# Kernel optimization log

Hardware: AMD Instinct MI355X
Metric: run time of the kernel (lower is better)

## Reference

```python
import jax, jax.numpy as jnp
import numpy as np

N = 50000
E = 800000
D = 128
L = 2


def setup_inputs() -> dict:
    key = jax.random.key(0)
    k0, k1, k2 = jax.random.split(key, 3)
    x = jax.random.normal(k0, (N, D), dtype=jnp.float32)
    edge_index = jax.random.randint(k1, (2, E), 0, N, dtype=jnp.int64)
    # GCNConv weights: one [D, D] matrix + bias per layer (dim_in -> dim_in)
    W = jax.random.normal(k2, (L, D, D), dtype=jnp.float32) * (1.0 / np.sqrt(D))
    b = jnp.zeros((L, D), dtype=jnp.float32)
    return {"x": x, "edge_index": edge_index, "W": W, "b": b}


def reference(x, edge_index, W, b):
    """Stacked GCNConv + relu (dropout is identity in eval mode).

    GCNConv: out = D^{-1/2} (A + I) D^{-1/2} (X W) + b, with self-loops added.
    """
    n = x.shape[0]
    loops = jnp.arange(n, dtype=edge_index.dtype)
    src = jnp.concatenate([edge_index[0], loops])  # [E + N]
    dst = jnp.concatenate([edge_index[1], loops])  # [E + N]
    # Degree (with self-loops) based symmetric normalization
    deg = jax.ops.segment_sum(jnp.ones_like(dst, dtype=x.dtype), dst, num_segments=n)
    dinv = jax.lax.rsqrt(deg)  # deg >= 1 thanks to self-loops
    coef = (dinv[src] * dinv[dst])[:, None]  # [E + N, 1]

    num_layers = W.shape[0]
    for i in range(num_layers):
        h = x @ W[i]  # transform first, as PyG GCNConv does
        x = jax.ops.segment_sum(h[src] * coef, dst, num_segments=n) + b[i]
        x = jax.nn.relu(x)
        # F.dropout with training=False is identity
    return x
```

## Files before the change

kernel.cpp:

```cpp
#include <hip/hip_runtime.h>
#include <hip/hip_fp16.h>


#define D 128
#define SCAN_B 256
#define WP 136
#define ABI 6

typedef _Float16 half8 __attribute__((ext_vector_type(8)));
typedef float floatx4 __attribute__((ext_vector_type(4)));


__global__ void count_kernel(const int* __restrict__ dst, int* deg8,
                             int* __restrict__ rank, int e, int n) {
    int i = blockIdx.x * blockDim.x + threadIdx.x;
    int c = (blockIdx.x & 7) * n;
    if (i < e) rank[i] = atomicAdd(&deg8[c + dst[i]], 1);
}

__global__ __launch_bounds__(256) void scanA_cvtw_kernel(const int* __restrict__ deg8,
                                                         int* __restrict__ degT,
                                                         int* __restrict__ base8,
                                                         int* __restrict__ partial,
                                                         int n, int nbs,
                                                         const float* __restrict__ W,
                                                         __half* __restrict__ WhT) {
    __shared__ int red[4];
    int tid = threadIdx.x;
    int bid = blockIdx.x;
    if (bid < nbs) {
        int i = bid * 256 + tid;
        int tot = 0;
        if (i < n) {
            int run = 0;
#pragma unroll
            for (int c = 0; c < 8; ++c) {
                base8[c * n + i] = run;
                run += deg8[c * n + i];
            }
            degT[i] = run;
            tot = run;
        }
        for (int off = 32; off > 0; off >>= 1) tot += __shfl_down(tot, off, 64);
        if ((tid & 63) == 0) red[tid >> 6] = tot;
        __syncthreads();
        if (tid == 0) partial[bid] = red[0] + red[1] + red[2] + red[3];
    } else {
        int id = (bid - nbs) * 256 + tid;
        int l = id >> 14;
        int rem = id & 16383;
        int f = rem >> 7;
        int k = rem & 127;
        WhT[id] = __float2half(W[l * 16384 + k * 128 + f]);
    }
}

__global__ __launch_bounds__(256) void scanB_kernel(const int* __restrict__ partial,
                                                    int* __restrict__ blockoff, int nb) {
    __shared__ int sc[256];
    int tid = threadIdx.x;
    int c = (tid < nb) ? partial[tid] : 0;
    sc[tid] = c;
    __syncthreads();
    for (int off = 1; off < 256; off <<= 1) {
        int v = (tid >= off) ? sc[tid - off] : 0;
        __syncthreads();
        sc[tid] += v;
        __syncthreads();
    }
    if (tid <= nb) blockoff[tid] = (tid == 0) ? 0 : sc[tid - 1];
}

__global__ __launch_bounds__(SCAN_B) void scanC_kernel(const int* __restrict__ degT,
                                                       const int* __restrict__ blockoff,
                                                       int* __restrict__ row_ptr,
                                                       float* __restrict__ dinv,
                                                       int n, int nb) {
    __shared__ int sc[SCAN_B];
    int tid = threadIdx.x;
    int i = blockIdx.x * SCAN_B + tid;
    int c = (i < n) ? degT[i] : 0;
    sc[tid] = c;
    __syncthreads();
    for (int off = 1; off < SCAN_B; off <<= 1) {
        int v = (tid >= off) ? sc[tid - off] : 0;
        __syncthreads();
        sc[tid] += v;
        __syncthreads();
    }
    if (i < n) {
        int base = blockoff[blockIdx.x] + sc[tid] - c;
        row_ptr[i] = base;
        dinv[i] = rsqrtf((float)(c + 1));
    }
    if (blockIdx.x == 0 && tid == 0) row_ptr[n] = blockoff[nb];
}


__device__ inline void gemm_body(int bid, int tid,
                                 const float* __restrict__ Xf,
                                 const __half* __restrict__ Xh,
                                 const __half* __restrict__ WhT,
                                 __half* __restrict__ Hh, int n, int fromFloat,
                                 _Float16* wlds) {
#pragma unroll
    for (int q = 0; q < 8; ++q) {
        int idx = tid + q * 256;
        int row = idx >> 4;
        int col8 = (idx & 15) * 8;
        const uint2* gsrc = (const uint2*)(WhT + row * 128 + col8);
        uint2 a = gsrc[0];
        uint2 b = gsrc[1];
        uint2* ldst = (uint2*)(wlds + row * WP + col8);
        ldst[0] = a;
        ldst[1] = b;
    }
    __syncthreads();

    const int wave = tid >> 6;
    const int lane = tid & 63;
    const int m = lane & 15;
    const int quad = lane >> 4;

    const int node = bid * 64 + wave * 16 + m;
    const int node_ld = node < n ? node : (n - 1);

    half8 bfr[4];
    if (fromFloat) {
#pragma unroll
        for (int k = 0; k < 4; ++k) {
            const float4* p = (const float4*)(Xf + (size_t)node_ld * 128 + k * 32 + quad * 8);
            float4 lo = p[0];
            float4 hi = p[1];
            half8 h;
            h[0] = (_Float16)lo.x; h[1] = (_Float16)lo.y;
            h[2] = (_Float16)lo.z; h[3] = (_Float16)lo.w;
            h[4] = (_Float16)hi.x; h[5] = (_Float16)hi.y;
            h[6] = (_Float16)hi.z; h[7] = (_Float16)hi.w;
            bfr[k] = h;
        }
    } else {
#pragma unroll
        for (int k = 0; k < 4; ++k) {
            bfr[k] = *(const half8*)(Xh + (size_t)node_ld * 128 + k * 32 + quad * 8);
        }
    }

    floatx4 acc[8];
#pragma unroll
    for (int f = 0; f < 8; ++f) acc[f] = (floatx4){0.f, 0.f, 0.f, 0.f};

#pragma unroll
    for (int f = 0; f < 8; ++f) {
#pragma unroll
        for (int k = 0; k < 4; ++k) {
            half8 a = *(const half8*)(wlds + (f * 16 + m) * WP + k * 32 + quad * 8);
            acc[f] = __builtin_amdgcn_mfma_f32_16x16x32_f16(a, bfr[k], acc[f], 0, 0, 0);
        }
    }

    if (node < n) {
#pragma unroll
        for (int f = 0; f < 8; ++f) {
            __half2 p0 = __floats2half2_rn(acc[f][0], acc[f][1]);
            __half2 p1 = __floats2half2_rn(acc[f][2], acc[f][3]);
            uint2 pk;
            pk.x = *(unsigned int*)&p0;
            pk.y = *(unsigned int*)&p1;
            *(uint2*)(Hh + (size_t)node * 128 + f * 16 + quad * 4) = pk;
        }
    }
}

__device__ inline void fill_body(int i,
                                 const int* __restrict__ src,
                                 const int* __restrict__ dst,
                                 const int* __restrict__ rank,
                                 const int* __restrict__ row_ptr,
                                 const int* __restrict__ base8,
                                 const float* __restrict__ dinv,
                                 int2* __restrict__ recs, int e, int n) {
    if (i < e) {
        int d = dst[i];
        int s = src[i];
        int c = (i >> 8) & 7;
        int pos = row_ptr[d] + base8[c * n + d] + rank[i];
        int2 rec;
        rec.x = s;
        rec.y = __float_as_int(dinv[s] * dinv[d]);
        recs[pos] = rec;
    }
}


__global__ __launch_bounds__(256) void gemmfill_kernel(const float* __restrict__ Xf,
                                                       const __half* __restrict__ WhT,
                                                       __half* __restrict__ Hh, int n, int nbg,
                                                       const int* __restrict__ src,
                                                       const int* __restrict__ dst,
                                                       const int* __restrict__ rank,
                                                       const int* __restrict__ row_ptr,
                                                       const int* __restrict__ base8,
                                                       const float* __restrict__ dinv,
                                                       int2* __restrict__ recs, int e) {
    __shared__ _Float16 wlds[128 * WP];
    int bid = blockIdx.x;
    int tid = threadIdx.x;
    if (bid < nbg) {
        gemm_body(bid, tid, Xf, nullptr, WhT, Hh, n, 1, wlds);
    } else {
        fill_body((bid - nbg) * 256 + tid, src, dst, rank, row_ptr, base8, dinv, recs, e, n);
    }
}

__global__ __launch_bounds__(256) void gemm_f16in_kernel(const __half* __restrict__ Xh,
                                                         const __half* __restrict__ WhT,
                                                         __half* __restrict__ Hh, int n) {
    __shared__ _Float16 wlds[128 * WP];
    gemm_body(blockIdx.x, threadIdx.x, nullptr, Xh, WhT, Hh, n, 0, wlds);
}


__device__ inline void unpack8(uint4 u, float* f) {
    union { unsigned int x; __half2 h; } a, b, c, d;
    a.x = u.x; b.x = u.y; c.x = u.z; d.x = u.w;
    float2 f0 = __half22float2(a.h);
    float2 f1 = __half22float2(b.h);
    float2 f2 = __half22float2(c.h);
    float2 f3 = __half22float2(d.h);
    f[0] = f0.x; f[1] = f0.y; f[2] = f1.x; f[3] = f1.y;
    f[4] = f2.x; f[5] = f2.y; f[6] = f3.x; f[7] = f3.y;
}

__global__ __launch_bounds__(256) void agg_kernel(const __half* __restrict__ H,
                                                  const int2* __restrict__ recs,
                                                  const int* __restrict__ row_ptr,
                                                  const float* __restrict__ dinv,
                                                  const float* __restrict__ bias,
                                                  float* __restrict__ YF,
                                                  __half* __restrict__ YH,
                                                  int n, int writeHalf) {
    int wave = threadIdx.x >> 6;
    int lane = threadIdx.x & 63;
    int v = blockIdx.x * 4 + wave;
    if (v >= n) return;

    const int qw = lane >> 4;
    const int fl = lane & 15;
    const uint4* H16 = (const uint4*)H;

    float acc[8];
    {
        float di = dinv[v];
        float selfc = (qw == 0) ? di * di : 0.f;
        uint4 hv = H16[(size_t)v * 16 + fl];
        float f[8]; unpack8(hv, f);
#pragma unroll
        for (int t = 0; t < 8; ++t) acc[t] = f[t] * selfc;
    }

    int e0 = row_ptr[v];
    int e1 = row_ptr[v + 1];
    int e = e0;
    for (; e + 4 * ABI <= e1; e += 4 * ABI) {
        int2 r[ABI]; uint4 hu[ABI];
#pragma unroll
        for (int j = 0; j < ABI; ++j) r[j] = recs[e + 4 * j + qw];
#pragma unroll
        for (int j = 0; j < ABI; ++j) hu[j] = H16[(size_t)r[j].x * 16 + fl];
#pragma unroll
        for (int j = 0; j < ABI; ++j) {
            float c = __int_as_float(r[j].y);
            float f[8]; unpack8(hu[j], f);
#pragma unroll
            for (int t = 0; t < 8; ++t) acc[t] = fmaf(f[t], c, acc[t]);
        }
    }
    if (e < e1) {
        int2 r[ABI]; uint4 hu[ABI]; bool act[ABI];
#pragma unroll
        for (int j = 0; j < ABI; ++j) {
            int idx = e + 4 * j + qw;
            act[j] = idx < e1;
            if (act[j]) r[j] = recs[idx];
        }
#pragma unroll
        for (int j = 0; j < ABI; ++j) {
            if (act[j]) hu[j] = H16[(size_t)r[j].x * 16 + fl];
        }
#pragma unroll
        for (int j = 0; j < ABI; ++j) {
            if (act[j]) {
                float c = __int_as_float(r[j].y);
                float f[8]; unpack8(hu[j], f);
#pragma unroll
                for (int t = 0; t < 8; ++t) acc[t] = fmaf(f[t], c, acc[t]);
            }
        }
    }

#pragma unroll
    for (int t = 0; t < 8; ++t) {
        acc[t] += __shfl_xor(acc[t], 16);
        acc[t] += __shfl_xor(acc[t], 32);
    }

    if (qw == 0) {
        const float4* B4 = (const float4*)bias;
        float4 b0 = B4[fl * 2];
        float4 b1 = B4[fl * 2 + 1];
        float o[8];
        o[0] = fmaxf(acc[0] + b0.x, 0.f);
        o[1] = fmaxf(acc[1] + b0.y, 0.f);
        o[2] = fmaxf(acc[2] + b0.z, 0.f);
        o[3] = fmaxf(acc[3] + b0.w, 0.f);
        o[4] = fmaxf(acc[4] + b1.x, 0.f);
        o[5] = fmaxf(acc[5] + b1.y, 0.f);
        o[6] = fmaxf(acc[6] + b1.z, 0.f);
        o[7] = fmaxf(acc[7] + b1.w, 0.f);
        if (writeHalf) {
            __half2 p0 = __floats2half2_rn(o[0], o[1]);
            __half2 p1 = __floats2half2_rn(o[2], o[3]);
            __half2 p2 = __floats2half2_rn(o[4], o[5]);
            __half2 p3 = __floats2half2_rn(o[6], o[7]);
            uint4 pk;
            pk.x = *(unsigned int*)&p0;
            pk.y = *(unsigned int*)&p1;
            pk.z = *(unsigned int*)&p2;
            pk.w = *(unsigned int*)&p3;
            ((uint4*)YH)[(size_t)v * 16 + fl] = pk;
        } else {
            float4* Y4 = (float4*)YF;
            Y4[(size_t)v * 32 + fl * 2]     = make_float4(o[0], o[1], o[2], o[3]);
            Y4[(size_t)v * 32 + fl * 2 + 1] = make_float4(o[4], o[5], o[6], o[7]);
        }
    }
}


extern "C" void kernel_launch(void* const* d_in, const int* in_sizes, int n_in,
                              void* d_out, int out_size, void* d_ws, size_t ws_size,
                              hipStream_t stream) {
    const float* x = (const float*)d_in[0];
    const int* ei = (const int*)d_in[1];
    const float* W = (const float*)d_in[2];
    const float* b = (const float*)d_in[3];
    float* out = (float*)d_out;

    const int N = in_sizes[0] / D;
    const int E = in_sizes[1] / 2;

    const int* src = ei;
    const int* dst = ei + E;

    int* wsi = (int*)d_ws;
    float* wsf = (float*)d_ws;
    const size_t o_deg8 = 0;
    const size_t o_degT = o_deg8 + 400000;
    const size_t o_dinv = o_degT + 50000;
    const size_t o_rp   = o_dinv + 50000;
    const size_t o_part = o_rp + 50016;
    const size_t o_boff = o_part + 256;
    const size_t o_b8   = o_boff + 256;
    const size_t o_rank = o_b8 + 400000;
    const size_t o_rec  = o_rank + 800000;
    const size_t o_h    = o_rec + 1600000;
    const size_t o_wht  = o_h + 3200000;
    const size_t o_y1h  = o_wht + 16384;

    int* deg8    = wsi + o_deg8;
    int* degT    = wsi + o_degT;
    float* dinv  = wsf + o_dinv;
    int* row_ptr = wsi + o_rp;
    int* partial = wsi + o_part;
    int* blockoff= wsi + o_boff;
    int* base8   = wsi + o_b8;
    int* rank    = wsi + o_rank;
    int2* recs   = (int2*)(wsi + o_rec);
    __half* h    = (__half*)(wsi + o_h);
    __half* wht  = (__half*)(wsi + o_wht);
    __half* y1h  = (__half*)(wsi + o_y1h);

    const int nb_e = (E + 255) / 256;
    const int nb_s = (N + SCAN_B - 1) / SCAN_B;
    const int nb_g = (N + 63) / 64;
    const int nb_a = (N + 3) / 4;

    hipMemsetAsync(deg8, 0, (size_t)8 * 50000 * sizeof(int), stream);
    count_kernel<<<nb_e, 256, 0, stream>>>(dst, deg8, rank, E, N);
    scanA_cvtw_kernel<<<nb_s + 128, 256, 0, stream>>>(deg8, degT, base8, partial,
                                                      N, nb_s, W, wht);
    scanB_kernel<<<1, 256, 0, stream>>>(partial, blockoff, nb_s);
    scanC_kernel<<<nb_s, SCAN_B, 0, stream>>>(degT, blockoff, row_ptr, dinv, N, nb_s);
    gemmfill_kernel<<<nb_g + nb_e, 256, 0, stream>>>(x, wht, h, N, nb_g,
                                                     src, dst, rank, row_ptr, base8,
                                                     dinv, recs, E);
    agg_kernel<<<nb_a, 256, 0, stream>>>(h, recs, row_ptr, dinv, b, nullptr, y1h, N, 1);
    gemm_f16in_kernel<<<nb_g, 256, 0, stream>>>(y1h, wht + 16384, h, N);
    agg_kernel<<<nb_a, 256, 0, stream>>>(h, recs, row_ptr, dinv, b + D, out, nullptr, N, 0);
}
```

Before: 238.4 us.

## Fuse deg zeroing with weight conversion, overlap first GEMM with edge counting

Replaces the memset with a zeroing kernel that also converts W to fp16 transposed. The first-layer GEMM now runs in the same launch as the atomic degree count instead of alongside the CSR fill, so the fill becomes its own kernel. This reorders the preprocessing schedule to hide the GEMM behind the atomic-bound count phase and removes one launch. In exchange, the count blocks now share a launch with GEMM blocks that need large LDS, which may limit occupancy for the atomic work.

```diff
diff --git a/kernel.cpp b/kernel.cpp
--- a/kernel.cpp
+++ b/kernel.cpp
@@ -11,48 +11,144 @@
 typedef float floatx4 __attribute__((ext_vector_type(4)));
 
 
-__global__ void count_kernel(const int* __restrict__ dst, int* deg8,
-                             int* __restrict__ rank, int e, int n) {
-    int i = blockIdx.x * blockDim.x + threadIdx.x;
-    int c = (blockIdx.x & 7) * n;
-    if (i < e) rank[i] = atomicAdd(&deg8[c + dst[i]], 1);
-}
-
-__global__ __launch_bounds__(256) void scanA_cvtw_kernel(const int* __restrict__ deg8,
-                                                         int* __restrict__ degT,
-                                                         int* __restrict__ base8,
-                                                         int* __restrict__ partial,
-                                                         int n, int nbs,
-                                                         const float* __restrict__ W,
-                                                         __half* __restrict__ WhT) {
-    __shared__ int red[4];
+__global__ __launch_bounds__(256) void zero_cvtw_kernel(int* __restrict__ deg8,
+                                                        int total4, int nzb,
+                                                        const float* __restrict__ W,
+                                                        __half* __restrict__ WhT) {
+    int bid = blockIdx.x;
     int tid = threadIdx.x;
-    int bid = blockIdx.x;
-    if (bid < nbs) {
+    if (bid < nzb) {
         int i = bid * 256 + tid;
-        int tot = 0;
-        if (i < n) {
-            int run = 0;
-#pragma unroll
-            for (int c = 0; c < 8; ++c) {
-                base8[c * n + i] = run;
-                run += deg8[c * n + i];
-            }
-            degT[i] = run;
-            tot = run;
-        }
-        for (int off = 32; off > 0; off >>= 1) tot += __shfl_down(tot, off, 64);
-        if ((tid & 63) == 0) red[tid >> 6] = tot;
-        __syncthreads();
-        if (tid == 0) partial[bid] = red[0] + red[1] + red[2] + red[3];
+        if (i < total4) ((int4*)deg8)[i] = make_int4(0, 0, 0, 0);
     } else {
-        int id = (bid - nbs) * 256 + tid;
+        int id = (bid - nzb) * 256 + tid;
         int l = id >> 14;
         int rem = id & 16383;
         int f = rem >> 7;
         int k = rem & 127;
         WhT[id] = __float2half(W[l * 16384 + k * 128 + f]);
     }
+}
+
+
+__device__ inline void gemm_body(int bid, int tid,
+                                 const float* __restrict__ Xf,
+                                 const __half* __restrict__ Xh,
+                                 const __half* __restrict__ WhT,
+                                 __half* __restrict__ Hh, int n, int fromFloat,
+                                 _Float16* wlds) {
+#pragma unroll
+    for (int q = 0; q < 8; ++q) {
+        int idx = tid + q * 256;
+        int row = idx >> 4;
+        int col8 = (idx & 15) * 8;
+        const uint2* gsrc = (const uint2*)(WhT + row * 128 + col8);
+        uint2 a = gsrc[0];
+        uint2 b = gsrc[1];
+        uint2* ldst = (uint2*)(wlds + row * WP + col8);
+        ldst[0] = a;
+        ldst[1] = b;
+    }
+    __syncthreads();
+
+    const int wave = tid >> 6;
+    const int lane = tid & 63;
+    const int m = lane & 15;
+    const int quad = lane >> 4;
+
+    const int node = bid * 64 + wave * 16 + m;
+    const int node_ld = node < n ? node : (n - 1);
+
+    half8 bfr[4];
+    if (fromFloat) {
+#pragma unroll
+        for (int k = 0; k < 4; ++k) {
+            const float4* p = (const float4*)(Xf + (size_t)node_ld * 128 + k * 32 + quad * 8);
+            float4 lo = p[0];
+            float4 hi = p[1];
+            half8 h;
+            h[0] = (_Float16)lo.x; h[1] = (_Float16)lo.y;
+            h[2] = (_Float16)lo.z; h[3] = (_Float16)lo.w;
+            h[4] = (_Float16)hi.x; h[5] = (_Float16)hi.y;
+            h[6] = (_Float16)hi.z; h[7] = (_Float16)hi.w;
+            bfr[k] = h;
+        }
+    } else {
+#pragma unroll
+        for (int k = 0; k < 4; ++k) {
+            bfr[k] = *(const half8*)(Xh + (size_t)node_ld * 128 + k * 32 + quad * 8);
+        }
+    }
+
+    floatx4 acc[8];
+#pragma unroll
+    for (int f = 0; f < 8; ++f) acc[f] = (floatx4){0.f, 0.f, 0.f, 0.f};
+
+#pragma unroll
+    for (int f = 0; f < 8; ++f) {
+#pragma unroll
+        for (int k = 0; k < 4; ++k) {
+            half8 a = *(const half8*)(wlds + (f * 16 + m) * WP + k * 32 + quad * 8);
+            acc[f] = __builtin_amdgcn_mfma_f32_16x16x32_f16(a, bfr[k], acc[f], 0, 0, 0);
+        }
+    }
+
+    if (node < n) {
+#pragma unroll
+        for (int f = 0; f < 8; ++f) {
+            __half2 p0 = __floats2half2_rn(acc[f][0], acc[f][1]);
+            __half2 p1 = __floats2half2_rn(acc[f][2], acc[f][3]);
+            uint2 pk;
+            pk.x = *(unsigned int*)&p0;
+            pk.y = *(unsigned int*)&p1;
+            *(uint2*)(Hh + (size_t)node * 128 + f * 16 + quad * 4) = pk;
+        }
+    }
+}
+
+
+__global__ __launch_bounds__(256) void count_gemm_kernel(const int* __restrict__ dst,
+                                                         int* deg8,
+                                                         int* __restrict__ rank,
+                                                         int e, int n, int nbe,
+                                                         const float* __restrict__ Xf,
+                                                         const __half* __restrict__ WhT,
+                                                         __half* __restrict__ Hh) {
+    __shared__ _Float16 wlds[128 * WP];
+    int bid = blockIdx.x;
+    int tid = threadIdx.x;
+    if (bid < nbe) {
+        int i = bid * 256 + tid;
+        int c = (bid & 7) * n;
+        if (i < e) rank[i] = atomicAdd(&deg8[c + dst[i]], 1);
+    } else {
+        gemm_body(bid - nbe, tid, Xf, nullptr, WhT, Hh, n, 1, wlds);
+    }
+}
+
+
+__global__ __launch_bounds__(256) void scanA_kernel(const int* __restrict__ deg8,
+                                                    int* __restrict__ degT,
+                                                    int* __restrict__ base8,
+                                                    int* __restrict__ partial, int n) {
+    __shared__ int red[4];
+    int tid = threadIdx.x;
+    int i = blockIdx.x * 256 + tid;
+    int tot = 0;
+    if (i < n) {
+        int run = 0;
+#pragma unroll
+        for (int c = 0; c < 8; ++c) {
+            base8[c * n + i] = run;
+            run += deg8[c * n + i];
+        }
+        degT[i] = run;
+        tot = run;
+    }
+    for (int off = 32; off > 0; off >>= 1) tot += __shfl_down(tot, off, 64);
+    if ((tid & 63) == 0) red[tid >> 6] = tot;
+    __syncthreads();
+    if (tid == 0) partial[blockIdx.x] = red[0] + red[1] + red[2] + red[3];
 }
 
 __global__ __launch_bounds__(256) void scanB_kernel(const int* __restrict__ partial,
@@ -97,89 +193,13 @@
 }
 
 
-__device__ inline void gemm_body(int bid, int tid,
-                                 const float* __restrict__ Xf,
-                                 const __half* __restrict__ Xh,
-                                 const __half* __restrict__ WhT,
-                                 __half* __restrict__ Hh, int n, int fromFloat,
-                                 _Float16* wlds) {
-#pragma unroll
-    for (int q = 0; q < 8; ++q) {
-        int idx = tid + q * 256;
-        int row = idx >> 4;
-        int col8 = (idx & 15) * 8;
-        const uint2* gsrc = (const uint2*)(WhT + row * 128 + col8);
-        uint2 a = gsrc[0];
-        uint2 b = gsrc[1];
-        uint2* ldst = (uint2*)(wlds + row * WP + col8);
-        ldst[0] = a;
-        ldst[1] = b;
-    }
-    __syncthreads();
-
-    const int wave = tid >> 6;
-    const int lane = tid & 63;
-    const int m = lane & 15;
-    const int quad = lane >> 4;
-
-    const int node = bid * 64 + wave * 16 + m;
-    const int node_ld = node < n ? node : (n - 1);
-
-    half8 bfr[4];
-    if (fromFloat) {
-#pragma unroll
-        for (int k = 0; k < 4; ++k) {
-            const float4* p = (const float4*)(Xf + (size_t)node_ld * 128 + k * 32 + quad * 8);
-            float4 lo = p[0];
-            float4 hi = p[1];
-            half8 h;
-            h[0] = (_Float16)lo.x; h[1] = (_Float16)lo.y;
-            h[2] = (_Float16)lo.z; h[3] = (_Float16)lo.w;
-            h[4] = (_Float16)hi.x; h[5] = (_Float16)hi.y;
-            h[6] = (_Float16)hi.z; h[7] = (_Float16)hi.w;
-            bfr[k] = h;
-        }
-    } else {
-#pragma unroll
-        for (int k = 0; k < 4; ++k) {
-            bfr[k] = *(const half8*)(Xh + (size_t)node_ld * 128 + k * 32 + quad * 8);
-        }
-    }
-
-    floatx4 acc[8];
-#pragma unroll
-    for (int f = 0; f < 8; ++f) acc[f] = (floatx4){0.f, 0.f, 0.f, 0.f};
-
-#pragma unroll
-    for (int f = 0; f < 8; ++f) {
-#pragma unroll
-        for (int k = 0; k < 4; ++k) {
-            half8 a = *(const half8*)(wlds + (f * 16 + m) * WP + k * 32 + quad * 8);
-            acc[f] = __builtin_amdgcn_mfma_f32_16x16x32_f16(a, bfr[k], acc[f], 0, 0, 0);
-        }
-    }
-
-    if (node < n) {
-#pragma unroll
-        for (int f = 0; f < 8; ++f) {
-            __half2 p0 = __floats2half2_rn(acc[f][0], acc[f][1]);
-            __half2 p1 = __floats2half2_rn(acc[f][2], acc[f][3]);
-            uint2 pk;
-            pk.x = *(unsigned int*)&p0;
-            pk.y = *(unsigned int*)&p1;
-            *(uint2*)(Hh + (size_t)node * 128 + f * 16 + quad * 4) = pk;
-        }
-    }
-}
-
-__device__ inline void fill_body(int i,
-                                 const int* __restrict__ src,
-                                 const int* __restrict__ dst,
-                                 const int* __restrict__ rank,
-                                 const int* __restrict__ row_ptr,
-                                 const int* __restrict__ base8,
-                                 const float* __restrict__ dinv,
-                                 int2* __restrict__ recs, int e, int n) {
+__global__ void fill_kernel(const int* __restrict__ src, const int* __restrict__ dst,
+                            const int* __restrict__ rank,
+                            const int* __restrict__ row_ptr,
+                            const int* __restrict__ base8,
+                            const float* __restrict__ dinv,
+                            int2* __restrict__ recs, int e, int n) {
+    int i = blockIdx.x * blockDim.x + threadIdx.x;
     if (i < e) {
         int d = dst[i];
         int s = src[i];
@@ -192,26 +212,6 @@
     }
 }
 
-
-__global__ __launch_bounds__(256) void gemmfill_kernel(const float* __restrict__ Xf,
-                                                       const __half* __restrict__ WhT,
-                                                       __half* __restrict__ Hh, int n, int nbg,
-                                                       const int* __restrict__ src,
-                                                       const int* __restrict__ dst,
-                                                       const int* __restrict__ rank,
-                                                       const int* __restrict__ row_ptr,
-                                                       const int* __restrict__ base8,
-                                                       const float* __restrict__ dinv,
-                                                       int2* __restrict__ recs, int e) {
-    __shared__ _Float16 wlds[128 * WP];
-    int bid = blockIdx.x;
-    int tid = threadIdx.x;
-    if (bid < nbg) {
-        gemm_body(bid, tid, Xf, nullptr, WhT, Hh, n, 1, wlds);
-    } else {
-        fill_body((bid - nbg) * 256 + tid, src, dst, rank, row_ptr, base8, dinv, recs, e, n);
-    }
-}
 
 __global__ __launch_bounds__(256) void gemm_f16in_kernel(const __half* __restrict__ Xh,
                                                          const __half* __restrict__ WhT,
@@ -385,16 +385,15 @@
     const int nb_s = (N + SCAN_B - 1) / SCAN_B;
     const int nb_g = (N + 63) / 64;
     const int nb_a = (N + 3) / 4;
-
-    hipMemsetAsync(deg8, 0, (size_t)8 * 50000 * sizeof(int), stream);
-    count_kernel<<<nb_e, 256, 0, stream>>>(dst, deg8, rank, E, N);
-    scanA_cvtw_kernel<<<nb_s + 128, 256, 0, stream>>>(deg8, degT, base8, partial,
-                                                      N, nb_s, W, wht);
+    const int nzb  = (100000 + 255) / 256;
+
+    zero_cvtw_kernel<<<nzb + 128, 256, 0, stream>>>(deg8, 100000, nzb, W, wht);
+    count_gemm_kernel<<<nb_e + nb_g, 256, 0, stream>>>(dst, deg8, rank, E, N, nb_e,
+                                                       x, wht, h);
+    scanA_kernel<<<nb_s, 256, 0, stream>>>(deg8, degT, base8, partial, N);
     scanB_kernel<<<1, 256, 0, stream>>>(partial, blockoff, nb_s);
     scanC_kernel<<<nb_s, SCAN_B, 0, stream>>>(degT, blockoff, row_ptr, dinv, N, nb_s);
-    gemmfill_kernel<<<nb_g + nb_e, 256, 0, stream>>>(x, wht, h, N, nb_g,
-                                                     src, dst, rank, row_ptr, base8,
-                                                     dinv, recs, E);
+    fill_kernel<<<nb_e, 256, 0, stream>>>(src, dst, rank, row_ptr, base8, dinv, recs, E, N);
     agg_kernel<<<nb_a, 256, 0, stream>>>(h, recs, row_ptr, dinv, b, nullptr, y1h, N, 1);
     gemm_f16in_kernel<<<nb_g, 256, 0, stream>>>(y1h, wht + 16384, h, N);
     agg_kernel<<<nb_a, 256, 0, stream>>>(h, recs, row_ptr, dinv, b + D, out, nullptr, N, 0);
```

After: 240.1 us. About the same (+0.8%).

## Slice feature matrix into 16-column panels and split aggregation across slices

Applied to the files above, without the earlier changes.

The intermediate H and Y1 matrices are stored as eight column slices of 16 halves each (slice-major), written that way by the GEMM and read that way by the next GEMM. Aggregation now launches eight blocks per node group, each handling one 16-column slice, so each gathered row is a 32-byte segment from a slice that is 1.6MB. The intent is to make each slice's working set cache-resident and raise edge-level parallelism. The cost is that the edge records are re-read eight times per node and there are more, smaller gathers.

```diff
diff --git a/kernel.cpp b/kernel.cpp
--- a/kernel.cpp
+++ b/kernel.cpp
@@ -5,7 +5,7 @@
 #define D 128
 #define SCAN_B 256
 #define WP 136
-#define ABI 6
+#define AB2 4
 
 typedef _Float16 half8 __attribute__((ext_vector_type(8)));
 typedef float floatx4 __attribute__((ext_vector_type(4)));
@@ -142,7 +142,8 @@
     } else {
 #pragma unroll
         for (int k = 0; k < 4; ++k) {
-            bfr[k] = *(const half8*)(Xh + (size_t)node_ld * 128 + k * 32 + quad * 8);
+            int sl = 2 * k + (quad >> 1);
+            bfr[k] = *(const half8*)(Xh + ((size_t)sl * n + node_ld) * 16 + (quad & 1) * 8);
         }
     }
 
@@ -167,7 +168,7 @@
             uint2 pk;
             pk.x = *(unsigned int*)&p0;
             pk.y = *(unsigned int*)&p1;
-            *(uint2*)(Hh + (size_t)node * 128 + f * 16 + quad * 4) = pk;
+            *(uint2*)(Hh + ((size_t)f * n + node) * 16 + quad * 4) = pk;
         }
     }
 }
@@ -221,17 +222,6 @@
 }
 
 
-__device__ inline void unpack8(uint4 u, float* f) {
-    union { unsigned int x; __half2 h; } a, b, c, d;
-    a.x = u.x; b.x = u.y; c.x = u.z; d.x = u.w;
-    float2 f0 = __half22float2(a.h);
-    float2 f1 = __half22float2(b.h);
-    float2 f2 = __half22float2(c.h);
-    float2 f3 = __half22float2(d.h);
-    f[0] = f0.x; f[1] = f0.y; f[2] = f1.x; f[3] = f1.y;
-    f[4] = f2.x; f[5] = f2.y; f[6] = f3.x; f[7] = f3.y;
-}
-
 __global__ __launch_bounds__(256) void agg_kernel(const __half* __restrict__ H,
                                                   const int2* __restrict__ recs,
                                                   const int* __restrict__ row_ptr,
@@ -242,97 +232,84 @@
                                                   int n, int writeHalf) {
     int wave = threadIdx.x >> 6;
     int lane = threadIdx.x & 63;
-    int v = blockIdx.x * 4 + wave;
+    int s = blockIdx.x & 7;
+    int v = (blockIdx.x >> 3) * 4 + wave;
     if (v >= n) return;
 
-    const int qw = lane >> 4;
-    const int fl = lane & 15;
-    const uint4* H16 = (const uint4*)H;
-
-    float acc[8];
+    const int eo = lane >> 3;
+    const int fl = lane & 7;
+    const unsigned int* Hu = (const unsigned int*)H;
+    const size_t sbase = (size_t)s * n;
+
+    float ax, ay;
     {
         float di = dinv[v];
-        float selfc = (qw == 0) ? di * di : 0.f;
-        uint4 hv = H16[(size_t)v * 16 + fl];
-        float f[8]; unpack8(hv, f);
-#pragma unroll
-        for (int t = 0; t < 8; ++t) acc[t] = f[t] * selfc;
+        float selfc = (eo == 0) ? di * di : 0.f;
+        union { unsigned int u; __half2 h; } cv;
+        cv.u = Hu[(sbase + v) * 8 + fl];
+        float2 hv = __half22float2(cv.h);
+        ax = hv.x * selfc;
+        ay = hv.y * selfc;
     }
 
     int e0 = row_ptr[v];
     int e1 = row_ptr[v + 1];
+    const unsigned long long* rec8 = (const unsigned long long*)recs;
     int e = e0;
-    for (; e + 4 * ABI <= e1; e += 4 * ABI) {
-        int2 r[ABI]; uint4 hu[ABI];
-#pragma unroll
-        for (int j = 0; j < ABI; ++j) r[j] = recs[e + 4 * j + qw];
-#pragma unroll
-        for (int j = 0; j < ABI; ++j) hu[j] = H16[(size_t)r[j].x * 16 + fl];
-#pragma unroll
-        for (int j = 0; j < ABI; ++j) {
-            float c = __int_as_float(r[j].y);
-            float f[8]; unpack8(hu[j], f);
-#pragma unroll
-            for (int t = 0; t < 8; ++t) acc[t] = fmaf(f[t], c, acc[t]);
+    for (; e + 8 * AB2 <= e1; e += 8 * AB2) {
+        unsigned long long r[AB2]; unsigned int hu[AB2];
+#pragma unroll
+        for (int j = 0; j < AB2; ++j)
+            r[j] = __builtin_nontemporal_load(rec8 + e + 8 * j + eo);
+#pragma unroll
+        for (int j = 0; j < AB2; ++j)
+            hu[j] = Hu[(sbase + (unsigned int)(r[j] & 0xffffffffu)) * 8 + fl];
+#pragma unroll
+        for (int j = 0; j < AB2; ++j) {
+            float c = __int_as_float((int)(r[j] >> 32));
+            union { unsigned int u; __half2 h; } t; t.u = hu[j];
+            float2 hs = __half22float2(t.h);
+            ax = fmaf(hs.x, c, ax);
+            ay = fmaf(hs.y, c, ay);
         }
     }
     if (e < e1) {
-        int2 r[ABI]; uint4 hu[ABI]; bool act[ABI];
-#pragma unroll
-        for (int j = 0; j < ABI; ++j) {
-            int idx = e + 4 * j + qw;
+        unsigned long long r[AB2]; unsigned int hu[AB2]; bool act[AB2];
+#pragma unroll
+        for (int j = 0; j < AB2; ++j) {
+            int idx = e + 8 * j + eo;
             act[j] = idx < e1;
-            if (act[j]) r[j] = recs[idx];
-        }
-#pragma unroll
-        for (int j = 0; j < ABI; ++j) {
-            if (act[j]) hu[j] = H16[(size_t)r[j].x * 16 + fl];
-        }
-#pragma unroll
-        for (int j = 0; j < ABI; ++j) {
+            if (act[j]) r[j] = __builtin_nontemporal_load(rec8 + idx);
+        }
+#pragma unroll
+        for (int j = 0; j < AB2; ++j) {
+            if (act[j]) hu[j] = Hu[(sbase + (unsigned int)(r[j] & 0xffffffffu)) * 8 + fl];
+        }
+#pragma unroll
+        for (int j = 0; j < AB2; ++j) {
             if (act[j]) {
-                float c = __int_as_float(r[j].y);
-                float f[8]; unpack8(hu[j], f);
-#pragma unroll
-                for (int t = 0; t < 8; ++t) acc[t] = fmaf(f[t], c, acc[t]);
+                float c = __int_as_float((int)(r[j] >> 32));
+                union { unsigned int u; __half2 h; } t; t.u = hu[j];
+                float2 hs = __half22float2(t.h);
+                ax = fmaf(hs.x, c, ax);
+                ay = fmaf(hs.y, c, ay);
             }
         }
     }
 
-#pragma unroll
-    for (int t = 0; t < 8; ++t) {
-        acc[t] += __shfl_xor(acc[t], 16);
-        acc[t] += __shfl_xor(acc[t], 32);
-    }
-
-    if (qw == 0) {
-        const float4* B4 = (const float4*)bias;
-        float4 b0 = B4[fl * 2];
-        float4 b1 = B4[fl * 2 + 1];
-        float o[8];
-        o[0] = fmaxf(acc[0] + b0.x, 0.f);
-        o[1] = fmaxf(acc[1] + b0.y, 0.f);
-        o[2] = fmaxf(acc[2] + b0.z, 0.f);
-        o[3] = fmaxf(acc[3] + b0.w, 0.f);
-        o[4] = fmaxf(acc[4] + b1.x, 0.f);
-        o[5] = fmaxf(acc[5] + b1.y, 0.f);
-        o[6] = fmaxf(acc[6] + b1.z, 0.f);
-        o[7] = fmaxf(acc[7] + b1.w, 0.f);
+    ax += __shfl_xor(ax, 8);  ay += __shfl_xor(ay, 8);
+    ax += __shfl_xor(ax, 16); ay += __shfl_xor(ay, 16);
+    ax += __shfl_xor(ax, 32); ay += __shfl_xor(ay, 32);
+
+    if (eo == 0) {
+        float2 bv = ((const float2*)bias)[s * 8 + fl];
+        float ox = fmaxf(ax + bv.x, 0.f);
+        float oy = fmaxf(ay + bv.y, 0.f);
         if (writeHalf) {
-            __half2 p0 = __floats2half2_rn(o[0], o[1]);
-            __half2 p1 = __floats2half2_rn(o[2], o[3]);
-            __half2 p2 = __floats2half2_rn(o[4], o[5]);
-            __half2 p3 = __floats2half2_rn(o[6], o[7]);
-            uint4 pk;
-            pk.x = *(unsigned int*)&p0;
-            pk.y = *(unsigned int*)&p1;
-            pk.z = *(unsigned int*)&p2;
-            pk.w = *(unsigned int*)&p3;
-            ((uint4*)YH)[(size_t)v * 16 + fl] = pk;
+            __half2 p = __floats2half2_rn(ox, oy);
+            ((unsigned int*)YH)[(sbase + v) * 8 + fl] = *(unsigned int*)&p;
         } else {
-            float4* Y4 = (float4*)YF;
-            Y4[(size_t)v * 32 + fl * 2]     = make_float4(o[0], o[1], o[2], o[3]);
-            Y4[(size_t)v * 32 + fl * 2 + 1] = make_float4(o[4], o[5], o[6], o[7]);
+            ((float2*)YF)[(size_t)v * 64 + s * 8 + fl] = make_float2(ox, oy);
         }
     }
 }
@@ -384,7 +361,7 @@
     const int nb_e = (E + 255) / 256;
     const int nb_s = (N + SCAN_B - 1) / SCAN_B;
     const int nb_g = (N + 63) / 64;
-    const int nb_a = (N + 3) / 4;
+    const int nb_a = ((N + 3) / 4) * 8;
 
     hipMemsetAsync(deg8, 0, (size_t)8 * 50000 * sizeof(int), stream);
     count_kernel<<<nb_e, 256, 0, stream>>>(dst, deg8, rank, E, N);
```

New measurement: 444.0 us. 86.3% more time.
